# Kernel optimization log

Measured on AMD Instinct MI355X. Metric: run time of the kernel, lower is better.

## Reference

```python
import jax, jax.numpy as jnp
import numpy as np
from jax import lax

K = 3
PAD = 1


def setup_inputs() -> dict:
    key = jax.random.key(0)
    k1, k2, k3 = jax.random.split(key, 3)
    B, Cin, Cout, H, W = 4, 64, 64, 128, 128
    x = jax.random.normal(k1, (B, Cin, H, W), dtype=jnp.float32)
    # offset-predicting conv params (2*K*K output channels); small init keeps offsets modest
    offset_w = jax.random.normal(k2, (2 * K * K, Cin, K, K), dtype=jnp.float32) * 0.05
    offset_b = jnp.zeros((2 * K * K,), dtype=jnp.float32)
    # deformable conv weight/bias (module uses randn weight, zero bias)
    weight = jax.random.normal(k3, (Cout, Cin, K, K), dtype=jnp.float32) * 0.05
    bias = jnp.zeros((Cout,), dtype=jnp.float32)
    return {"x": x, "offset_w": offset_w, "offset_b": offset_b, "weight": weight, "bias": bias}


def _conv2d(x, w, b):
    y = lax.conv_general_dilated(x, w, window_strides=(1, 1),
                                 padding=((PAD, PAD), (PAD, PAD)),
                                 dimension_numbers=("NCHW", "OIHW", "NCHW"))
    return y + b[None, :, None, None]


def _bilinear_gather(x, py, px):
    # x: [B,C,H,W]; py,px: [B,KK,HO,WO] sample coords -> [B,C,KK,HO,WO], zeros outside
    B, C, H, W = x.shape
    y0 = jnp.floor(py)
    x0 = jnp.floor(px)
    ly = py - y0
    lx = px - x0
    y0i = y0.astype(jnp.int32)
    x0i = x0.astype(jnp.int32)
    xf = x.reshape(B, C, H * W)

    def corner(yi, xi, w):
        mask = ((yi >= 0) & (yi < H) & (xi >= 0) & (xi < W)).astype(x.dtype)
        lin = jnp.clip(yi, 0, H - 1) * W + jnp.clip(xi, 0, W - 1)  # [B,KK,HO,WO]
        g = jax.vmap(lambda xb, ib: xb[:, ib])(xf, lin)            # [B,C,KK,HO,WO]
        return g * (w * mask)[:, None]

    return (corner(y0i, x0i, (1 - ly) * (1 - lx))
            + corner(y0i, x0i + 1, (1 - ly) * lx)
            + corner(y0i + 1, x0i, ly * (1 - lx))
            + corner(y0i + 1, x0i + 1, ly * lx))


def reference(x, offset_w, offset_b, weight, bias):
    B, Cin, H, W = x.shape
    Cout = weight.shape[0]
    KK = K * K
    offset = _conv2d(x, offset_w, offset_b)            # [B, 2*KK, H, W]
    off = offset.reshape(B, KK, 2, H, W)               # torchvision layout: (dy, dx) per tap
    dy, dx = off[:, :, 0], off[:, :, 1]                # [B,KK,H,W]
    ki = (jnp.arange(KK) // K).astype(x.dtype)
    kj = (jnp.arange(KK) % K).astype(x.dtype)
    hs = jnp.arange(H, dtype=x.dtype)
    ws = jnp.arange(W, dtype=x.dtype)
    base_y = ki[:, None, None] + hs[None, :, None] - PAD   # [KK,H,1]
    base_x = kj[:, None, None] + ws[None, None, :] - PAD   # [KK,1,W]
    py = dy + base_y[None]                             # [B,KK,H,W]
    px = dx + base_x[None]
    sampled = _bilinear_gather(x, py, px)              # [B,Cin,KK,H,W]
    out = jnp.einsum("bckhw,ock->bohw", sampled, weight.reshape(Cout, Cin, KK))
    return out + bias[None, :, None, None]
```

## Files before the change

kernel.cpp:

```cpp
#include <hip/hip_runtime.h>

typedef _Float16 f16x8 __attribute__((ext_vector_type(8)));
typedef float f32x4 __attribute__((ext_vector_type(4)));

__device__ __forceinline__ f16x8 splat8(float v) {
  _Float16 h = (_Float16)v;
  return f16x8{h, h, h, h, h, h, h, h};
}

__device__ __forceinline__ int swzh(int i) { return i ^ (((i >> 6) & 7) << 3); }

__global__ __launch_bounds__(256) void k_xtprep(const float* __restrict__ x,
                                                const float* __restrict__ wt,
                                                const float* __restrict__ ow,
                                                _Float16* __restrict__ xt,
                                                _Float16* __restrict__ wb,
                                                _Float16* __restrict__ owb) {
  __shared__ float tile[64 * 65];
  int blk = blockIdx.x;
  int t = threadIdx.x;
  if (blk < 1024) {
    int b = blk >> 8;
    int y = (blk >> 1) & 127;
    int w0 = (blk & 1) * 64;
    const float* xp = x + ((size_t)(b * 64) * 128 + y) * 128 + w0;
#pragma unroll
    for (int it = 0; it < 4; ++it) {
      int idx = it * 256 + t;
      int c = idx >> 4, q = idx & 15;
      float4 v = *(const float4*)(xp + (size_t)c * 16384 + q * 4);
      float* tp = &tile[c * 65 + q * 4];
      tp[0] = v.x; tp[1] = v.y; tp[2] = v.z; tp[3] = v.w;
    }
    __syncthreads();
#pragma unroll
    for (int it = 0; it < 2; ++it) {
      int idx = it * 256 + t;
      int w = idx >> 3, c8 = idx & 7;
      f16x8 o;
#pragma unroll
      for (int j = 0; j < 8; ++j) o[j] = (_Float16)tile[(c8 * 8 + j) * 65 + w];
      *(f16x8*)&xt[(((size_t)b * 128 + y) * 128 + w0 + w) * 64 + c8 * 8] = o;
    }
  } else {
    int i = (blk - 1024) * 256 + t;
    if (i < 36864) {
      int k = i >> 12, rem = i & 4095, o = rem >> 6, c = rem & 63;
      wb[i] = (_Float16)wt[(o * 64 + c) * 9 + k];
    } else if (i < 36864 + 18432) {
      int j = i - 36864;
      int k = j >> 11, rem = j & 2047, o = rem >> 6, c = rem & 63;
      float v = (o < 18) ? ow[(o * 64 + c) * 9 + k] : 0.0f;
      owb[j] = (_Float16)v;
    }
  }
}

__global__ __launch_bounds__(256, 4) void k_fused(
    const _Float16* __restrict__ xt, const _Float16* __restrict__ wb,
    const _Float16* __restrict__ owb, const float* __restrict__ ob,
    const float* __restrict__ bias, float* __restrict__ out) {
  __shared__ char lds[40960];
  _Float16* Sb = (_Float16*)lds;
  _Float16* Wp = (_Float16*)(lds + 16384);
  _Float16* Xs = (_Float16*)lds;
  _Float16* owbp = (_Float16*)(lds + 32768);
  float* offL = (float*)(lds + 32768);

  int t = threadIdx.x;
  int lb = (blockIdx.x & 7) * 128 + (blockIdx.x >> 3);
  int w0 = (lb & 1) * 64;
  int h = (lb >> 1) & 127;
  int b = lb >> 8;

  int lane = t & 63, wid = t >> 6;
  int row = lane & 15, quad = lane >> 4;
  const _Float16* xb = xt + (size_t)b * 128 * 128 * 64;

#pragma unroll
  for (int it = 0; it < 8; ++it) {
    int idx8 = it * 256 + t;
    if (idx8 < 1584) {
      int c8 = idx8 & 7;
      int jr = idx8 >> 3;
      int jj = jr % 66;
      int ki = jr / 66;
      int gy = h - 1 + ki;
      int gx = w0 - 1 + jj;
      f16x8 v = {};
      if (((unsigned)gy < 128u) & ((unsigned)gx < 128u))
        v = *(const f16x8*)(xb + ((size_t)gy * 128 + gx) * 64 + c8 * 8);
      *(f16x8*)&Xs[(ki * 66 + jj) * 72 + c8 * 8] = v;
    } else if (idx8 < 1840) {
      int j = idx8 - 1584;
      int o = j >> 3, c8 = j & 7;
      *(f16x8*)&owbp[swzh(o * 64 + c8 * 8)] = *(const f16x8*)(owb + j * 8);
    }
  }
  __syncthreads();

  {
    int woA = (wid >> 1) * 16;
    int wpA = (wid & 1) * 32;
    f32x4 accA[2];
    accA[0] = f32x4{0.f, 0.f, 0.f, 0.f};
    accA[1] = f32x4{0.f, 0.f, 0.f, 0.f};
#pragma unroll
    for (int k = 0; k < 9; ++k) {
      if (k < 8) {
        int o = t >> 3, c8 = t & 7;
        f16x8 v = *(const f16x8*)(owb + (k + 1) * 2048 + t * 8);
        *(f16x8*)&owbp[swzh(((k + 1) & 1) * 2048 + o * 64 + c8 * 8)] = v;
      }
      int ki = k / 3, kj = k % 3;
      int ai = (k & 1) * 2048 + (woA + row) * 64 + quad * 8;
      f16x8 afr0 = *(const f16x8*)&owbp[swzh(ai)];
      f16x8 afr1 = *(const f16x8*)&owbp[swzh(ai + 32)];
#pragma unroll
      for (int n = 0; n < 2; ++n) {
        int j = wpA + n * 16 + row + kj;
        const _Float16* lp = &Xs[(ki * 66 + j) * 72 + quad * 8];
        f16x8 b0 = *(const f16x8*)(lp);
        f16x8 b1 = *(const f16x8*)(lp + 32);
        accA[n] = __builtin_amdgcn_mfma_f32_16x16x32_f16(afr0, b0, accA[n], 0, 0, 0);
        accA[n] = __builtin_amdgcn_mfma_f32_16x16x32_f16(afr1, b1, accA[n], 0, 0, 0);
      }
      __syncthreads();
    }
    int qr = quad * 4;
#pragma unroll
    for (int n = 0; n < 2; ++n) {
#pragma unroll
      for (int r = 0; r < 4; ++r) {
        int co = woA + qr + r;
        if (co < 18)
          offL[(wpA + n * 16 + row) * 20 + co] = accA[n][r] + ob[co];
      }
    }
  }
  __syncthreads();

  int pix = t >> 2, cg = t & 3;
  int w = w0 + pix;
  int woB = (wid >> 1) * 32, wpB = (wid & 1) * 32;

  f16x8 wk0, wk1, ga0, ga1, gb0, gb1, gc0, gc1, gd0, gd1;
  float w00, w01, w10, w11;

#define SAMPLE_ISSUE(KK)                                                     \
  {                                                                          \
    float dy = offL[pix * 20 + 2 * (KK)];                                    \
    float dx = offL[pix * 20 + 2 * (KK) + 1];                                \
    float py = dy + (float)(h + (KK) / 3 - 1);                               \
    float pxf = dx + (float)(w + (KK) % 3 - 1);                              \
    float fy = floorf(py), fx = floorf(pxf);                                 \
    float ly = py - fy, lx = pxf - fx;                                       \
    int y0 = (int)fy, x0 = (int)fx;                                          \
    int y1 = y0 + 1, x1 = x0 + 1;                                            \
    bool vy0 = (unsigned)y0 < 128u, vy1 = (unsigned)y1 < 128u;               \
    bool vx0 = (unsigned)x0 < 128u, vx1 = (unsigned)x1 < 128u;               \
    w00 = (vy0 && vx0) ? (1.f - ly) * (1.f - lx) : 0.f;                      \
    w01 = (vy0 && vx1) ? (1.f - ly) * lx : 0.f;                              \
    w10 = (vy1 && vx0) ? ly * (1.f - lx) : 0.f;                              \
    w11 = (vy1 && vx1) ? ly * lx : 0.f;                                      \
    int yc0 = min(max(y0, 0), 127), yc1 = min(max(y1, 0), 127);              \
    int xc0 = min(max(x0, 0), 127), xc1 = min(max(x1, 0), 127);              \
    const _Float16* p00 = xb + (yc0 * 128 + xc0) * 64 + cg * 16;             \
    int dxo = (xc1 - xc0) * 64, dyo = (yc1 - yc0) * 8192;                    \
    ga0 = *(const f16x8*)(p00);                                              \
    ga1 = *(const f16x8*)(p00 + 8);                                          \
    gb0 = *(const f16x8*)(p00 + dxo);                                        \
    gb1 = *(const f16x8*)(p00 + dxo + 8);                                    \
    gc0 = *(const f16x8*)(p00 + dyo);                                        \
    gc1 = *(const f16x8*)(p00 + dyo + 8);                                    \
    gd0 = *(const f16x8*)(p00 + dyo + dxo);                                  \
    gd1 = *(const f16x8*)(p00 + dyo + dxo + 8);                              \
  }

#define SAMPLE_FINISH(DSTBUF)                                                \
  {                                                                          \
    f16x8 W00 = splat8(w00), W01 = splat8(w01);                              \
    f16x8 W10 = splat8(w10), W11 = splat8(w11);                              \
    f16x8 s0 = W00 * ga0 + W01 * gb0 + W10 * gc0 + W11 * gd0;                \
    f16x8 s1 = W00 * ga1 + W01 * gb1 + W10 * gc1 + W11 * gd1;                \
    int si = (DSTBUF) * 4096 + pix * 64 + cg * 16;                           \
    *(f16x8*)&Sb[swzh(si)] = s0;                                             \
    *(f16x8*)&Sb[swzh(si + 8)] = s1;                                         \
  }

  f32x4 acc[2][2];
#pragma unroll
  for (int i = 0; i < 2; ++i)
#pragma unroll
    for (int j = 0; j < 2; ++j) acc[i][j] = f32x4{0.f, 0.f, 0.f, 0.f};

  {
    const f16x8* wsrc = (const f16x8*)wb;
    wk0 = wsrc[t];
    wk1 = wsrc[256 + t];
    SAMPLE_ISSUE(0)
    SAMPLE_FINISH(0)
    int wi = (t >> 3) * 64 + (t & 7) * 8;
    *(f16x8*)&Wp[swzh(wi)] = wk0;
    *(f16x8*)&Wp[swzh(wi + 2048)] = wk1;
  }
  __syncthreads();

#pragma unroll
  for (int k = 0; k < 9; ++k) {
    if (k < 8) {
      const f16x8* wsrc = (const f16x8*)(wb + (k + 1) * 4096);
      wk0 = wsrc[t];
      wk1 = wsrc[256 + t];
      SAMPLE_ISSUE(k + 1)
    }
    {
      int bufo = (k & 1) * 4096;
#pragma unroll
      for (int ks = 0; ks < 2; ++ks) {
        int c0 = ks * 32 + quad * 8;
        f16x8 afr[2], bfr[2];
#pragma unroll
        for (int mi = 0; mi < 2; ++mi)
          afr[mi] = *(const f16x8*)&Wp[swzh(bufo + (woB + mi * 16 + row) * 64 + c0)];
#pragma unroll
        for (int ni = 0; ni < 2; ++ni)
          bfr[ni] = *(const f16x8*)&Sb[swzh(bufo + (wpB + ni * 16 + row) * 64 + c0)];
#pragma unroll
        for (int mi = 0; mi < 2; ++mi)
#pragma unroll
          for (int ni = 0; ni < 2; ++ni)
            acc[mi][ni] = __builtin_amdgcn_mfma_f32_16x16x32_f16(
                afr[mi], bfr[ni], acc[mi][ni], 0, 0, 0);
      }
    }
    if (k < 8) {
      SAMPLE_FINISH((k + 1) & 1)
      int wi = ((k + 1) & 1) * 4096 + (t >> 3) * 64 + (t & 7) * 8;
      *(f16x8*)&Wp[swzh(wi)] = wk0;
      *(f16x8*)&Wp[swzh(wi + 2048)] = wk1;
      __syncthreads();
    }
  }
#undef SAMPLE_ISSUE
#undef SAMPLE_FINISH

  {
    int col = lane & 15;
    int qr = quad * 4;
#pragma unroll
    for (int mi = 0; mi < 2; ++mi) {
#pragma unroll
      for (int ni = 0; ni < 2; ++ni) {
#pragma unroll
        for (int r = 0; r < 4; ++r) {
          int o = woB + mi * 16 + qr + r;
          int pw = w0 + wpB + ni * 16 + col;
          out[(((size_t)b * 64 + o) * 128 + h) * 128 + pw] = acc[mi][ni][r] + bias[o];
        }
      }
    }
  }
}

extern "C" void kernel_launch(void* const* d_in, const int* in_sizes, int n_in,
                              void* d_out, int out_size, void* d_ws,
                              size_t ws_size, hipStream_t stream) {
  const float* x = (const float*)d_in[0];
  const float* ow = (const float*)d_in[1];
  const float* ob = (const float*)d_in[2];
  const float* wt = (const float*)d_in[3];
  const float* bias = (const float*)d_in[4];
  float* out = (float*)d_out;

  char* ws = (char*)d_ws;
  _Float16* xt = (_Float16*)ws;
  _Float16* wb = (_Float16*)(ws + 8388608);
  _Float16* owb = (_Float16*)(ws + 8388608 + 73728);

  k_xtprep<<<1240, 256, 0, stream>>>(x, wt, ow, xt, wb, owb);
  k_fused<<<1024, 256, 0, stream>>>(xt, wb, owb, ob, bias, out);
}
```

Measured before the change: 41.91 us.

## Load conv weight fragments directly from global into registers, drop LDS staging

Both the offset-conv weights and the main deformable-conv weights are now read straight from global memory into MFMA A-fragment registers, instead of being staged through double-buffered LDS. The LDS footprint shrinks and the per-tap syncthreads in the offset phase go away. The x tile is re-laid out with XOR swizzling at a 64-half stride instead of padding to 72. A sched_barrier is added so the next tap's weight and sample loads issue before the current tap's MFMAs. In exchange there are more global (L2) reads per wave and higher register pressure from the double-buffered weight fragments.

```diff
diff --git a/kernel.cpp b/kernel.cpp
--- a/kernel.cpp
+++ b/kernel.cpp
@@ -60,12 +60,10 @@
     const _Float16* __restrict__ xt, const _Float16* __restrict__ wb,
     const _Float16* __restrict__ owb, const float* __restrict__ ob,
     const float* __restrict__ bias, float* __restrict__ out) {
-  __shared__ char lds[40960];
+  __shared__ char lds[30464];
+  _Float16* Xs = (_Float16*)lds;
   _Float16* Sb = (_Float16*)lds;
-  _Float16* Wp = (_Float16*)(lds + 16384);
-  _Float16* Xs = (_Float16*)lds;
-  _Float16* owbp = (_Float16*)(lds + 32768);
-  float* offL = (float*)(lds + 32768);
+  float* offL = (float*)(lds + 25344);
 
   int t = threadIdx.x;
   int lb = (blockIdx.x & 7) * 128 + (blockIdx.x >> 3);
@@ -78,7 +76,7 @@
   const _Float16* xb = xt + (size_t)b * 128 * 128 * 64;
 
 #pragma unroll
-  for (int it = 0; it < 8; ++it) {
+  for (int it = 0; it < 7; ++it) {
     int idx8 = it * 256 + t;
     if (idx8 < 1584) {
       int c8 = idx8 & 7;
@@ -90,11 +88,7 @@
       f16x8 v = {};
       if (((unsigned)gy < 128u) & ((unsigned)gx < 128u))
         v = *(const f16x8*)(xb + ((size_t)gy * 128 + gx) * 64 + c8 * 8);
-      *(f16x8*)&Xs[(ki * 66 + jj) * 72 + c8 * 8] = v;
-    } else if (idx8 < 1840) {
-      int j = idx8 - 1584;
-      int o = j >> 3, c8 = j & 7;
-      *(f16x8*)&owbp[swzh(o * 64 + c8 * 8)] = *(const f16x8*)(owb + j * 8);
+      *(f16x8*)&Xs[swzh(jr * 64 + c8 * 8)] = v;
     }
   }
   __syncthreads();
@@ -107,25 +101,19 @@
     accA[1] = f32x4{0.f, 0.f, 0.f, 0.f};
 #pragma unroll
     for (int k = 0; k < 9; ++k) {
-      if (k < 8) {
-        int o = t >> 3, c8 = t & 7;
-        f16x8 v = *(const f16x8*)(owb + (k + 1) * 2048 + t * 8);
-        *(f16x8*)&owbp[swzh(((k + 1) & 1) * 2048 + o * 64 + c8 * 8)] = v;
-      }
       int ki = k / 3, kj = k % 3;
-      int ai = (k & 1) * 2048 + (woA + row) * 64 + quad * 8;
-      f16x8 afr0 = *(const f16x8*)&owbp[swzh(ai)];
-      f16x8 afr1 = *(const f16x8*)&owbp[swzh(ai + 32)];
+      const _Float16* ap = owb + k * 2048 + (woA + row) * 64 + quad * 8;
+      f16x8 afr0 = *(const f16x8*)(ap);
+      f16x8 afr1 = *(const f16x8*)(ap + 32);
 #pragma unroll
       for (int n = 0; n < 2; ++n) {
         int j = wpA + n * 16 + row + kj;
-        const _Float16* lp = &Xs[(ki * 66 + j) * 72 + quad * 8];
-        f16x8 b0 = *(const f16x8*)(lp);
-        f16x8 b1 = *(const f16x8*)(lp + 32);
+        int bi = (ki * 66 + j) * 64 + quad * 8;
+        f16x8 b0 = *(const f16x8*)&Xs[swzh(bi)];
+        f16x8 b1 = *(const f16x8*)&Xs[swzh(bi + 32)];
         accA[n] = __builtin_amdgcn_mfma_f32_16x16x32_f16(afr0, b0, accA[n], 0, 0, 0);
         accA[n] = __builtin_amdgcn_mfma_f32_16x16x32_f16(afr1, b1, accA[n], 0, 0, 0);
       }
-      __syncthreads();
     }
     int qr = quad * 4;
 #pragma unroll
@@ -144,8 +132,20 @@
   int w = w0 + pix;
   int woB = (wid >> 1) * 32, wpB = (wid & 1) * 32;
 
-  f16x8 wk0, wk1, ga0, ga1, gb0, gb1, gc0, gc1, gd0, gd1;
+  f16x8 wkA[4], wkB[4];
+  f16x8 ga0, ga1, gb0, gb1, gc0, gc1, gd0, gd1;
   float w00, w01, w10, w11;
+
+  int wfo = row * 64 + quad * 8;
+
+#define LOAD_WFRAG(KK, DST)                                                  \
+  {                                                                          \
+    const _Float16* wp_ = wb + (KK) * 4096 + woB * 64 + wfo;                 \
+    DST[0] = *(const f16x8*)(wp_);                                           \
+    DST[1] = *(const f16x8*)(wp_ + 32);                                      \
+    DST[2] = *(const f16x8*)(wp_ + 1024);                                    \
+    DST[3] = *(const f16x8*)(wp_ + 1024 + 32);                               \
+  }
 
 #define SAMPLE_ISSUE(KK)                                                     \
   {                                                                          \
@@ -188,62 +188,58 @@
     *(f16x8*)&Sb[swzh(si + 8)] = s1;                                         \
   }
 
+#define MFMA_TAP(BUF, WREG)                                                  \
+  {                                                                          \
+    int bufo = (BUF) * 4096;                                                 \
+    _Pragma("unroll") for (int ks = 0; ks < 2; ++ks) {                       \
+      int c0 = ks * 32 + quad * 8;                                           \
+      f16x8 bfr[2];                                                          \
+      _Pragma("unroll") for (int ni = 0; ni < 2; ++ni)                       \
+          bfr[ni] =                                                          \
+          *(const f16x8*)&Sb[swzh(bufo + (wpB + ni * 16 + row) * 64 + c0)];  \
+      _Pragma("unroll") for (int mi = 0; mi < 2; ++mi)                       \
+          _Pragma("unroll") for (int ni = 0; ni < 2; ++ni) acc[mi][ni] =     \
+          __builtin_amdgcn_mfma_f32_16x16x32_f16(WREG[mi * 2 + ks], bfr[ni], \
+                                                 acc[mi][ni], 0, 0, 0);      \
+  }                                                                          \
+  }
+
   f32x4 acc[2][2];
 #pragma unroll
   for (int i = 0; i < 2; ++i)
 #pragma unroll
     for (int j = 0; j < 2; ++j) acc[i][j] = f32x4{0.f, 0.f, 0.f, 0.f};
 
-  {
-    const f16x8* wsrc = (const f16x8*)wb;
-    wk0 = wsrc[t];
-    wk1 = wsrc[256 + t];
-    SAMPLE_ISSUE(0)
-    SAMPLE_FINISH(0)
-    int wi = (t >> 3) * 64 + (t & 7) * 8;
-    *(f16x8*)&Wp[swzh(wi)] = wk0;
-    *(f16x8*)&Wp[swzh(wi + 2048)] = wk1;
-  }
+  LOAD_WFRAG(0, wkA)
+  SAMPLE_ISSUE(0)
+  SAMPLE_FINISH(0)
   __syncthreads();
 
-#pragma unroll
-  for (int k = 0; k < 9; ++k) {
-    if (k < 8) {
-      const f16x8* wsrc = (const f16x8*)(wb + (k + 1) * 4096);
-      wk0 = wsrc[t];
-      wk1 = wsrc[256 + t];
-      SAMPLE_ISSUE(k + 1)
-    }
-    {
-      int bufo = (k & 1) * 4096;
-#pragma unroll
-      for (int ks = 0; ks < 2; ++ks) {
-        int c0 = ks * 32 + quad * 8;
-        f16x8 afr[2], bfr[2];
-#pragma unroll
-        for (int mi = 0; mi < 2; ++mi)
-          afr[mi] = *(const f16x8*)&Wp[swzh(bufo + (woB + mi * 16 + row) * 64 + c0)];
-#pragma unroll
-        for (int ni = 0; ni < 2; ++ni)
-          bfr[ni] = *(const f16x8*)&Sb[swzh(bufo + (wpB + ni * 16 + row) * 64 + c0)];
-#pragma unroll
-        for (int mi = 0; mi < 2; ++mi)
-#pragma unroll
-          for (int ni = 0; ni < 2; ++ni)
-            acc[mi][ni] = __builtin_amdgcn_mfma_f32_16x16x32_f16(
-                afr[mi], bfr[ni], acc[mi][ni], 0, 0, 0);
-      }
-    }
-    if (k < 8) {
-      SAMPLE_FINISH((k + 1) & 1)
-      int wi = ((k + 1) & 1) * 4096 + (t >> 3) * 64 + (t & 7) * 8;
-      *(f16x8*)&Wp[swzh(wi)] = wk0;
-      *(f16x8*)&Wp[swzh(wi + 2048)] = wk1;
-      __syncthreads();
-    }
-  }
+#define PHASEB_ITER(K, WCUR, WNXT)                                           \
+  {                                                                          \
+    LOAD_WFRAG((K) + 1, WNXT)                                                \
+    SAMPLE_ISSUE((K) + 1)                                                    \
+    __builtin_amdgcn_sched_barrier(0);                                       \
+    MFMA_TAP((K) & 1, WCUR)                                                  \
+    SAMPLE_FINISH(((K) + 1) & 1)                                             \
+    __syncthreads();                                                         \
+  }
+
+  PHASEB_ITER(0, wkA, wkB)
+  PHASEB_ITER(1, wkB, wkA)
+  PHASEB_ITER(2, wkA, wkB)
+  PHASEB_ITER(3, wkB, wkA)
+  PHASEB_ITER(4, wkA, wkB)
+  PHASEB_ITER(5, wkB, wkA)
+  PHASEB_ITER(6, wkA, wkB)
+  PHASEB_ITER(7, wkB, wkA)
+  MFMA_TAP(0, wkA)
+
+#undef PHASEB_ITER
+#undef MFMA_TAP
+#undef SAMPLE_FINISH
 #undef SAMPLE_ISSUE
-#undef SAMPLE_FINISH
+#undef LOAD_WFRAG
 
   {
     int col = lane & 15;
```

After: 53.11 us. 1.27x slower.
